# Performance work log

Hardware: AMD Instinct MI355X
Metric: run time of the kernel (lower is better)

Reference implementation:

```python
import jax, jax.numpy as jnp
import numpy as np

B, S, D, H = 8, 2048, 1024, 64

def setup_inputs() -> dict:
    key = jax.random.key(0)
    ks = jax.random.split(key, 7)
    scale = 0.02
    return {
        "x": jax.random.normal(ks[0], (B, S, D), dtype=jnp.float32),
        "Wq": jax.random.normal(ks[1], (D, H), dtype=jnp.float32) * scale,
        "bq": jax.random.normal(ks[2], (H,), dtype=jnp.float32) * scale,
        "Wk": jax.random.normal(ks[3], (D, H), dtype=jnp.float32) * scale,
        "bk": jax.random.normal(ks[4], (H,), dtype=jnp.float32) * scale,
        "Wv": jax.random.normal(ks[5], (D, H), dtype=jnp.float32) * scale,
        "bv": jax.random.normal(ks[6], (H,), dtype=jnp.float32) * scale,
    }

def reference(x, Wq, bq, Wk, bk, Wv, bv):
    # Single-head causal self-attention (dropout in eval mode -> identity).
    q = x @ Wq + bq            # [B,S,H]
    k = x @ Wk + bk            # [B,S,H]
    v = x @ Wv + bv            # [B,S,H]
    scores = jnp.einsum("bqh,bkh->bqk", q, k)  # [B,S,S]
    s = q.shape[1]
    causal = jnp.tril(jnp.ones((s, s), dtype=bool))
    # Original masks with -inf BEFORE scaling; -inf/scale == -inf, so equivalent.
    scores = jnp.where(causal, scores, -jnp.inf) / jnp.sqrt(jnp.float32(k.shape[-1]))
    attn = jax.nn.softmax(scores, axis=-1)
    return jnp.einsum("bqk,bkh->bqh", attn, v)
```

## Files before the change

kernel.cpp:

```cpp
#include <hip/hip_runtime.h>
#include <math.h>

#define BATCH 8
#define SEQ   2048
#define DIM   1024
#define HD    64
#define NROWS (BATCH * SEQ)
#define CHUNK 512
#define NCHUNK 4
#define QTILE 32
#define NQT   (SEQ / QTILE)

typedef __attribute__((ext_vector_type(8))) short bf16x8;
typedef __attribute__((ext_vector_type(4))) float f32x4;

__device__ __forceinline__ unsigned short f2bf(float f) {
    unsigned u = __float_as_uint(f);
    u = (u + 0x7FFFu + ((u >> 16) & 1u)) >> 16;
    return (unsigned short)u;
}

__device__ __forceinline__ void gld_lds16(const void* g, void* l) {
    __builtin_amdgcn_global_load_lds(
        (const __attribute__((address_space(1))) void*)g,
        (__attribute__((address_space(3))) void*)l, 16, 0, 0);
}

__global__ __launch_bounds__(256)
void prep_w_kernel(const float* __restrict__ Wq, const float* __restrict__ Wk,
                   const float* __restrict__ Wv, unsigned short* __restrict__ Wt)
{
    const int mat = blockIdx.y;
    const float* __restrict__ W = (mat == 0) ? Wq : (mat == 1) ? Wk : Wv;
    const int k0 = blockIdx.x * 64;
    __shared__ float T[64][65];
    const int t = threadIdx.x;
    #pragma unroll
    for (int i = 0; i < 16; ++i) {
        const int idx = t + i * 256;
        T[idx >> 6][idx & 63] = W[(size_t)(k0 + (idx >> 6)) * HD + (idx & 63)];
    }
    __syncthreads();
    const int n = t >> 2;
    const int c = t & 3;
    union { unsigned short h[16]; uint4 v[2]; } buf;
    #pragma unroll
    for (int j = 0; j < 16; ++j) buf.h[j] = f2bf(T[c * 16 + j][n]);
    unsigned short* dst = Wt + ((size_t)mat * HD + n) * DIM + k0 + c * 16;
    *(uint4*)dst       = buf.v[0];
    *(uint4*)(dst + 8) = buf.v[1];
}

__global__ __launch_bounds__(256)
void qkv_mfma_kernel(const float* __restrict__ x,
                     const unsigned short* __restrict__ Wt,
                     const float* __restrict__ bq, const float* __restrict__ bk,
                     const float* __restrict__ bv,
                     unsigned short* __restrict__ Qg,
                     unsigned short* __restrict__ Kg,
                     unsigned short* __restrict__ Vtg)
{
    __shared__ unsigned short Xs[32][64];
    __shared__ unsigned short Ws[192][64];

    const int t    = threadIdx.x;
    const int lane = t & 63;
    const int w    = t >> 6;
    const int col  = lane & 15;
    const int quad = lane >> 4;
    const int rh   = w & 1;
    const int chh  = w >> 1;
    const int row0 = blockIdx.x * 32;

    const int xr  = t >> 3,  xc  = t & 7;
    const int wrl = lane >> 3, wcl = lane & 7;

    f32x4 acc[6];
    #pragma unroll
    for (int i = 0; i < 6; ++i) acc[i] = (f32x4){0.f, 0.f, 0.f, 0.f};

    for (int k0 = 0; k0 < DIM; k0 += 64) {
        __syncthreads();
        #pragma unroll
        for (int ii = 0; ii < 6; ++ii) {
            const int rbase = w * 48 + ii * 8;
            gld_lds16(&Wt[(size_t)(rbase + wrl) * DIM + k0 + wcl * 8], &Ws[rbase][0]);
        }
        {
            const float* xp = &x[(size_t)(row0 + xr) * DIM + k0 + xc * 8];
            const float4 v0 = *(const float4*)xp;
            const float4 v1 = *(const float4*)(xp + 4);
            uint4 o;
            o.x = (unsigned)f2bf(v0.x) | ((unsigned)f2bf(v0.y) << 16);
            o.y = (unsigned)f2bf(v0.z) | ((unsigned)f2bf(v0.w) << 16);
            o.z = (unsigned)f2bf(v1.x) | ((unsigned)f2bf(v1.y) << 16);
            o.w = (unsigned)f2bf(v1.z) | ((unsigned)f2bf(v1.w) << 16);
            *(uint4*)&Xs[xr][xc * 8] = o;
        }
        __syncthreads();
        #pragma unroll
        for (int ks = 0; ks < 2; ++ks) {
            const bf16x8 a = *(const bf16x8*)&Xs[rh * 16 + col][ks * 32 + quad * 8];
            #pragma unroll
            for (int nt = 0; nt < 6; ++nt) {
                const bf16x8 b = *(const bf16x8*)&Ws[chh * 96 + nt * 16 + col][ks * 32 + quad * 8];
                acc[nt] = __builtin_amdgcn_mfma_f32_16x16x32_bf16(a, b, acc[nt], 0, 0, 0);
            }
        }
    }

    const int b    = row0 / SEQ;
    const int s0   = (row0 % SEQ) + rh * 16 + quad * 4;
    const int grow = row0 + rh * 16 + quad * 4;
    #pragma unroll
    for (int nt = 0; nt < 6; ++nt) {
        const int gcol = chh * 96 + nt * 16 + col;
        const int mat  = gcol >> 6;
        const int nn   = gcol & 63;
        const float bvv = ((mat == 0) ? bq : (mat == 1) ? bk : bv)[nn];
        if (mat < 2) {
            unsigned short* __restrict__ o = (mat == 0) ? Qg : Kg;
            #pragma unroll
            for (int r = 0; r < 4; ++r)
                o[(size_t)(grow + r) * HD + nn] = f2bf(acc[nt][r] + bvv);
        } else {
            const unsigned lo = (unsigned)f2bf(acc[nt][0] + bvv) | ((unsigned)f2bf(acc[nt][1] + bvv) << 16);
            const unsigned hi = (unsigned)f2bf(acc[nt][2] + bvv) | ((unsigned)f2bf(acc[nt][3] + bvv) << 16);
            *(uint2*)&Vtg[((size_t)b * HD + nn) * SEQ + s0] = make_uint2(lo, hi);
        }
    }
}

__global__ __launch_bounds__(128)
void attn_part_kernel(const unsigned short* __restrict__ Qg,
                      const unsigned short* __restrict__ Kg,
                      const unsigned short* __restrict__ Vtg,
                      float* __restrict__ Opart,
                      float* __restrict__ ML)
{
    const int xb = blockIdx.x;
    const int c  = xb >> 9;
    const int b  = (xb >> 6) & 7;
    const int qt = xb & 63;
    if (qt < c * 16) return;

    __shared__ unsigned short Ks[64][64];
    __shared__ unsigned short Vs[64][64];
    __shared__ unsigned short Ps[2][16][72];

    const int t    = threadIdx.x;
    const int w    = t >> 6;
    const int lane = t & 63;
    const int col  = lane & 15;
    const int quad = lane >> 4;
    const int q0w  = qt * QTILE + w * 16;
    const size_t gq = (size_t)b * SEQ + q0w;

    const bf16x8 aq0 = *(const bf16x8*)&Qg[(gq + col) * HD + quad * 8];
    const bf16x8 aq1 = *(const bf16x8*)&Qg[(gq + col) * HD + 32 + quad * 8];

    f32x4 oacc[4];
    #pragma unroll
    for (int n = 0; n < 4; ++n) oacc[n] = (f32x4){0.f, 0.f, 0.f, 0.f};
    float mrow[4], lrow[4];
    #pragma unroll
    for (int r = 0; r < 4; ++r) { mrow[r] = -INFINITY; lrow[r] = 0.f; }

    const int kbeg   = c * CHUNK;
    const int kend   = min((c + 1) * CHUNK, (qt + 1) * QTILE);
    const int ntiles = (kend - kbeg + 63) >> 6;

    const int srow = lane >> 3, sc8 = lane & 7;
    const unsigned short* kgb = Kg  + (size_t)b * SEQ * HD;
    const unsigned short* vgb = Vtg + (size_t)b * HD * SEQ;

    for (int it = 0; it < ntiles; ++it) {
        const int j0 = kbeg + it * 64;
        __syncthreads();
        #pragma unroll
        for (int ii = 0; ii < 4; ++ii) {
            const int rb = w * 32 + ii * 8;
            gld_lds16(&kgb[(size_t)(j0 + rb + srow) * HD + sc8 * 8], &Ks[rb][0]);
            gld_lds16(&vgb[(size_t)(rb + srow) * SEQ + j0 + sc8 * 8], &Vs[rb][0]);
        }
        __syncthreads();

        if (j0 <= q0w + 15) {
            f32x4 scv[4];
            #pragma unroll
            for (int nt = 0; nt < 4; ++nt) {
                const bf16x8 bk0 = *(const bf16x8*)&Ks[nt * 16 + col][quad * 8];
                const bf16x8 bk1 = *(const bf16x8*)&Ks[nt * 16 + col][32 + quad * 8];
                f32x4 s = __builtin_amdgcn_mfma_f32_16x16x32_bf16(aq0, bk0, (f32x4){0.f,0.f,0.f,0.f}, 0, 0, 0);
                s = __builtin_amdgcn_mfma_f32_16x16x32_bf16(aq1, bk1, s, 0, 0, 0);
                scv[nt] = s;
            }
            const bool needmask = (j0 + 63 > q0w);
            #pragma unroll
            for (int r = 0; r < 4; ++r) {
                const int row = q0w + quad * 4 + r;
                float sv[4];
                float tmax = -INFINITY;
                if (needmask) {
                    #pragma unroll
                    for (int nt = 0; nt < 4; ++nt) {
                        const int key = j0 + nt * 16 + col;
                        sv[nt] = (key <= row) ? scv[nt][r] * 0.125f : -INFINITY;
                        tmax = fmaxf(tmax, sv[nt]);
                    }
                } else {
                    #pragma unroll
                    for (int nt = 0; nt < 4; ++nt) {
                        sv[nt] = scv[nt][r] * 0.125f;
                        tmax = fmaxf(tmax, sv[nt]);
                    }
                }
                #pragma unroll
                for (int off = 1; off < 16; off <<= 1)
                    tmax = fmaxf(tmax, __shfl_xor(tmax, off, 64));
                const float mnew  = fmaxf(mrow[r], tmax);
                const float alpha = __expf(mrow[r] - mnew);
                mrow[r] = mnew;
                float psum = 0.f;
                #pragma unroll
                for (int nt = 0; nt < 4; ++nt) {
                    const float p = __expf(sv[nt] - mnew);
                    psum += p;
                    Ps[w][quad * 4 + r][nt * 16 + col] = f2bf(p);
                }
                #pragma unroll
                for (int off = 1; off < 16; off <<= 1)
                    psum += __shfl_xor(psum, off, 64);
                lrow[r] = lrow[r] * alpha + psum;
                #pragma unroll
                for (int n = 0; n < 4; ++n) oacc[n][r] *= alpha;
            }
            #pragma unroll
            for (int ks = 0; ks < 2; ++ks) {
                const bf16x8 ap = *(const bf16x8*)&Ps[w][col][ks * 32 + quad * 8];
                #pragma unroll
                for (int n = 0; n < 4; ++n) {
                    const bf16x8 bv2 = *(const bf16x8*)&Vs[n * 16 + col][ks * 32 + quad * 8];
                    oacc[n] = __builtin_amdgcn_mfma_f32_16x16x32_bf16(ap, bv2, oacc[n], 0, 0, 0);
                }
            }
        }
    }

    const int blk = (b * NQT + qt) * NCHUNK + c;
    float* Ob = Opart + (size_t)blk * (QTILE * HD);
    #pragma unroll
    for (int n = 0; n < 4; ++n)
        #pragma unroll
        for (int r = 0; r < 4; ++r)
            Ob[(w * 16 + quad * 4 + r) * HD + n * 16 + col] = oacc[n][r];
    if (col == 0) {
        float* mlb = ML + (size_t)blk * 64;
        #pragma unroll
        for (int r = 0; r < 4; ++r) {
            mlb[w * 16 + quad * 4 + r]      = mrow[r];
            mlb[32 + w * 16 + quad * 4 + r] = lrow[r];
        }
    }
}

__global__ __launch_bounds__(256)
void combine_kernel(const float* __restrict__ Opart,
                    const float* __restrict__ ML,
                    float* __restrict__ out)
{
    const int gid = blockIdx.x * 256 + threadIdx.x;
    const int i   = gid >> 6;
    const int d   = gid & 63;
    const int b   = i >> 11;
    const int s   = i & 2047;
    const int qt  = s >> 5;
    const int r32 = s & 31;
    const int nc  = (s >> 9) + 1;
    const int blk0 = (b * NQT + qt) * NCHUNK;

    float m[NCHUNK], l[NCHUNK];
    float M = -INFINITY;
    for (int cc = 0; cc < nc; ++cc) {
        m[cc] = ML[(size_t)(blk0 + cc) * 64 + r32];
        l[cc] = ML[(size_t)(blk0 + cc) * 64 + 32 + r32];
        M = fmaxf(M, m[cc]);
    }
    float L = 0.f, acc = 0.f;
    for (int cc = 0; cc < nc; ++cc) {
        const float e = __expf(m[cc] - M);
        L   += l[cc] * e;
        acc += e * Opart[(size_t)(blk0 + cc) * (QTILE * HD) + r32 * HD + d];
    }
    out[(size_t)i * HD + d] = acc / L;
}

extern "C" void kernel_launch(void* const* d_in, const int* in_sizes, int n_in,
                              void* d_out, int out_size, void* d_ws, size_t ws_size,
                              hipStream_t stream) {
    const float* x  = (const float*)d_in[0];
    const float* Wq = (const float*)d_in[1];
    const float* bq = (const float*)d_in[2];
    const float* Wk = (const float*)d_in[3];
    const float* bk = (const float*)d_in[4];
    const float* Wv = (const float*)d_in[5];
    const float* bv = (const float*)d_in[6];
    float* out = (float*)d_out;

    unsigned short* Wt  = (unsigned short*)d_ws;
    unsigned short* Qg  = Wt + (size_t)3 * HD * DIM;
    unsigned short* Kg  = Qg + (size_t)NROWS * HD;
    unsigned short* Vtg = Kg + (size_t)NROWS * HD;
    float* Opart = (float*)(Vtg + (size_t)BATCH * HD * SEQ);
    float* ML    = Opart + (size_t)BATCH * NQT * NCHUNK * QTILE * HD;

    prep_w_kernel<<<dim3(16, 3), 256, 0, stream>>>(Wq, Wk, Wv, Wt);
    qkv_mfma_kernel<<<dim3(NROWS / 32), 256, 0, stream>>>(x, Wt, bq, bk, bv, Qg, Kg, Vtg);
    attn_part_kernel<<<dim3(NCHUNK * BATCH * NQT), 128, 0, stream>>>(Qg, Kg, Vtg, Opart, ML);
    combine_kernel<<<dim3(NROWS * HD / 256), 256, 0, stream>>>(Opart, ML, out);
}
```

Before: 165.9 us.

## Swizzle LDS tiles, split attention into 8 key chunks, use 6-wave QKV blocks

Applies an XOR swizzle to the 16-byte column chunks of the X, W, K and V shared-memory tiles in the QKV projection and attention kernels. This is meant to remove LDS bank conflicts on the MFMA operand reads. It also halves the key chunk size to 256 with 8 chunks, giving the attention kernel more, shorter blocks for better load balance across the causal triangle. The cost is more partial outputs for the combine kernel to read and merge. The QKV kernel now uses 384 threads, one wave per (matrix, row-half) pair with 4 accumulator tiles, which lowers per-wave register use and simplifies the bias selection.

```diff
diff --git a/kernel.cpp b/kernel.cpp
--- a/kernel.cpp
+++ b/kernel.cpp
@@ -6,8 +6,8 @@
 #define DIM   1024
 #define HD    64
 #define NROWS (BATCH * SEQ)
-#define CHUNK 512
-#define NCHUNK 4
+#define CHUNK 256
+#define NCHUNK 8
 #define QTILE 32
 #define NQT   (SEQ / QTILE)
 
@@ -25,6 +25,7 @@
         (const __attribute__((address_space(1))) void*)g,
         (__attribute__((address_space(3))) void*)l, 16, 0, 0);
 }
+
 
 __global__ __launch_bounds__(256)
 void prep_w_kernel(const float* __restrict__ Wq, const float* __restrict__ Wk,
@@ -51,7 +52,7 @@
     *(uint4*)(dst + 8) = buf.v[1];
 }
 
-__global__ __launch_bounds__(256)
+__global__ __launch_bounds__(384)
 void qkv_mfma_kernel(const float* __restrict__ x,
                      const unsigned short* __restrict__ Wt,
                      const float* __restrict__ bq, const float* __restrict__ bk,
@@ -69,24 +70,26 @@
     const int col  = lane & 15;
     const int quad = lane >> 4;
     const int rh   = w & 1;
-    const int chh  = w >> 1;
+    const int mat  = w >> 1;
     const int row0 = blockIdx.x * 32;
 
-    const int xr  = t >> 3,  xc  = t & 7;
-    const int wrl = lane >> 3, wcl = lane & 7;
-
-    f32x4 acc[6];
-    #pragma unroll
-    for (int i = 0; i < 6; ++i) acc[i] = (f32x4){0.f, 0.f, 0.f, 0.f};
+    const int r8 = lane >> 3, ch = lane & 7;
+    const int xr = t >> 3,  xc = t & 7;
+
+    f32x4 acc[4];
+    #pragma unroll
+    for (int i = 0; i < 4; ++i) acc[i] = (f32x4){0.f, 0.f, 0.f, 0.f};
+
+    const int swzr = (ch ^ r8) * 8;
 
     for (int k0 = 0; k0 < DIM; k0 += 64) {
         __syncthreads();
         #pragma unroll
-        for (int ii = 0; ii < 6; ++ii) {
-            const int rbase = w * 48 + ii * 8;
-            gld_lds16(&Wt[(size_t)(rbase + wrl) * DIM + k0 + wcl * 8], &Ws[rbase][0]);
-        }
-        {
+        for (int ii = 0; ii < 4; ++ii) {
+            const int rbase = w * 32 + ii * 8;
+            gld_lds16(&Wt[(size_t)(rbase + r8) * DIM + k0 + swzr], &Ws[rbase][0]);
+        }
+        if (t < 256) {
             const float* xp = &x[(size_t)(row0 + xr) * DIM + k0 + xc * 8];
             const float4 v0 = *(const float4*)xp;
             const float4 v1 = *(const float4*)(xp + 4);
@@ -95,15 +98,16 @@
             o.y = (unsigned)f2bf(v0.z) | ((unsigned)f2bf(v0.w) << 16);
             o.z = (unsigned)f2bf(v1.x) | ((unsigned)f2bf(v1.y) << 16);
             o.w = (unsigned)f2bf(v1.z) | ((unsigned)f2bf(v1.w) << 16);
-            *(uint4*)&Xs[xr][xc * 8] = o;
+            *(uint4*)&Xs[xr][(xc ^ (xr & 7)) * 8] = o;
         }
         __syncthreads();
         #pragma unroll
         for (int ks = 0; ks < 2; ++ks) {
-            const bf16x8 a = *(const bf16x8*)&Xs[rh * 16 + col][ks * 32 + quad * 8];
-            #pragma unroll
-            for (int nt = 0; nt < 6; ++nt) {
-                const bf16x8 b = *(const bf16x8*)&Ws[chh * 96 + nt * 16 + col][ks * 32 + quad * 8];
+            const int fswz = ((ks * 4 + quad) ^ (col & 7)) * 8;
+            const bf16x8 a = *(const bf16x8*)&Xs[rh * 16 + col][fswz];
+            #pragma unroll
+            for (int nt = 0; nt < 4; ++nt) {
+                const bf16x8 b = *(const bf16x8*)&Ws[mat * 64 + nt * 16 + col][fswz];
                 acc[nt] = __builtin_amdgcn_mfma_f32_16x16x32_bf16(a, b, acc[nt], 0, 0, 0);
             }
         }
@@ -112,12 +116,11 @@
     const int b    = row0 / SEQ;
     const int s0   = (row0 % SEQ) + rh * 16 + quad * 4;
     const int grow = row0 + rh * 16 + quad * 4;
-    #pragma unroll
-    for (int nt = 0; nt < 6; ++nt) {
-        const int gcol = chh * 96 + nt * 16 + col;
-        const int mat  = gcol >> 6;
-        const int nn   = gcol & 63;
-        const float bvv = ((mat == 0) ? bq : (mat == 1) ? bk : bv)[nn];
+    const float* __restrict__ bias = (mat == 0) ? bq : (mat == 1) ? bk : bv;
+    #pragma unroll
+    for (int nt = 0; nt < 4; ++nt) {
+        const int nn = nt * 16 + col;
+        const float bvv = bias[nn];
         if (mat < 2) {
             unsigned short* __restrict__ o = (mat == 0) ? Qg : Kg;
             #pragma unroll
@@ -142,7 +145,7 @@
     const int c  = xb >> 9;
     const int b  = (xb >> 6) & 7;
     const int qt = xb & 63;
-    if (qt < c * 16) return;
+    if (qt < c * 8) return;
 
     __shared__ unsigned short Ks[64][64];
     __shared__ unsigned short Vs[64][64];
@@ -170,7 +173,8 @@
     const int kend   = min((c + 1) * CHUNK, (qt + 1) * QTILE);
     const int ntiles = (kend - kbeg + 63) >> 6;
 
-    const int srow = lane >> 3, sc8 = lane & 7;
+    const int r8 = lane >> 3, ch = lane & 7;
+    const int swzr = (ch ^ r8) * 8;
     const unsigned short* kgb = Kg  + (size_t)b * SEQ * HD;
     const unsigned short* vgb = Vtg + (size_t)b * HD * SEQ;
 
@@ -180,8 +184,8 @@
         #pragma unroll
         for (int ii = 0; ii < 4; ++ii) {
             const int rb = w * 32 + ii * 8;
-            gld_lds16(&kgb[(size_t)(j0 + rb + srow) * HD + sc8 * 8], &Ks[rb][0]);
-            gld_lds16(&vgb[(size_t)(rb + srow) * SEQ + j0 + sc8 * 8], &Vs[rb][0]);
+            gld_lds16(&kgb[(size_t)(j0 + rb + r8) * HD + swzr], &Ks[rb][0]);
+            gld_lds16(&vgb[(size_t)(rb + r8) * SEQ + j0 + swzr], &Vs[rb][0]);
         }
         __syncthreads();
 
@@ -189,8 +193,10 @@
             f32x4 scv[4];
             #pragma unroll
             for (int nt = 0; nt < 4; ++nt) {
-                const bf16x8 bk0 = *(const bf16x8*)&Ks[nt * 16 + col][quad * 8];
-                const bf16x8 bk1 = *(const bf16x8*)&Ks[nt * 16 + col][32 + quad * 8];
+                const int sw0 = (quad ^ (col & 7)) * 8;
+                const int sw1 = ((4 + quad) ^ (col & 7)) * 8;
+                const bf16x8 bk0 = *(const bf16x8*)&Ks[nt * 16 + col][sw0];
+                const bf16x8 bk1 = *(const bf16x8*)&Ks[nt * 16 + col][sw1];
                 f32x4 s = __builtin_amdgcn_mfma_f32_16x16x32_bf16(aq0, bk0, (f32x4){0.f,0.f,0.f,0.f}, 0, 0, 0);
                 s = __builtin_amdgcn_mfma_f32_16x16x32_bf16(aq1, bk1, s, 0, 0, 0);
                 scv[nt] = s;
@@ -238,9 +244,10 @@
             #pragma unroll
             for (int ks = 0; ks < 2; ++ks) {
                 const bf16x8 ap = *(const bf16x8*)&Ps[w][col][ks * 32 + quad * 8];
+                const int fswz = ((ks * 4 + quad) ^ (col & 7)) * 8;
                 #pragma unroll
                 for (int n = 0; n < 4; ++n) {
-                    const bf16x8 bv2 = *(const bf16x8*)&Vs[n * 16 + col][ks * 32 + quad * 8];
+                    const bf16x8 bv2 = *(const bf16x8*)&Vs[n * 16 + col][fswz];
                     oacc[n] = __builtin_amdgcn_mfma_f32_16x16x32_bf16(ap, bv2, oacc[n], 0, 0, 0);
                 }
             }
@@ -276,20 +283,18 @@
     const int s   = i & 2047;
     const int qt  = s >> 5;
     const int r32 = s & 31;
-    const int nc  = (s >> 9) + 1;
+    const int nc  = (s >> 8) + 1;
     const int blk0 = (b * NQT + qt) * NCHUNK;
 
-    float m[NCHUNK], l[NCHUNK];
     float M = -INFINITY;
-    for (int cc = 0; cc < nc; ++cc) {
-        m[cc] = ML[(size_t)(blk0 + cc) * 64 + r32];
-        l[cc] = ML[(size_t)(blk0 + cc) * 64 + 32 + r32];
-        M = fmaxf(M, m[cc]);
-    }
+    for (int cc = 0; cc < nc; ++cc)
+        M = fmaxf(M, ML[(size_t)(blk0 + cc) * 64 + r32]);
     float L = 0.f, acc = 0.f;
     for (int cc = 0; cc < nc; ++cc) {
-        const float e = __expf(m[cc] - M);
-        L   += l[cc] * e;
+        const float m = ML[(size_t)(blk0 + cc) * 64 + r32];
+        const float l = ML[(size_t)(blk0 + cc) * 64 + 32 + r32];
+        const float e = __expf(m - M);
+        L   += l * e;
         acc += e * Opart[(size_t)(blk0 + cc) * (QTILE * HD) + r32 * HD + d];
     }
     out[(size_t)i * HD + d] = acc / L;
@@ -315,7 +320,7 @@
     float* ML    = Opart + (size_t)BATCH * NQT * NCHUNK * QTILE * HD;
 
     prep_w_kernel<<<dim3(16, 3), 256, 0, stream>>>(Wq, Wk, Wv, Wt);
-    qkv_mfma_kernel<<<dim3(NROWS / 32), 256, 0, stream>>>(x, Wt, bq, bk, bv, Qg, Kg, Vtg);
+    qkv_mfma_kernel<<<dim3(NROWS / 32), 384, 0, stream>>>(x, Wt, bq, bk, bv, Qg, Kg, Vtg);
     attn_part_kernel<<<dim3(NCHUNK * BATCH * NQT), 128, 0, stream>>>(Qg, Kg, Vtg, Opart, ML);
     combine_kernel<<<dim3(NROWS * HD / 256), 256, 0, stream>>>(Opart, ML, out);
 }
```

New measurement: 160.1 us. 1.04x faster.
